# Kernel tuning notes

Hardware: AMD Instinct MI355X
Metric: run time of the kernel (lower is better)

The kernel has to match this reference:

```python
import jax, jax.numpy as jnp
import numpy as np

B = 4096
N_WIRES = 4
N_OPS = 8
# fixed (control, target) wire pairs for the 8 'random' two-qubit CRY gates
PAIRS = [(0, 1), (1, 2), (2, 3), (3, 0), (0, 2), (1, 3), (2, 0), (3, 1)]
AX = "abcd"  # einsum letters for the 4 qubit axes


def _cry(theta):
    """Controlled-RY gate as a [2,2,2,2] tensor (c_out, t_out, c_in, t_in). Real-valued."""
    c, s = jnp.cos(theta / 2), jnp.sin(theta / 2)
    ry = jnp.stack([jnp.stack([c, -s]), jnp.stack([s, c])])  # [2,2]
    G = jnp.zeros((2, 2, 2, 2), dtype=ry.dtype)
    G = G.at[0, :, 0, :].set(jnp.eye(2, dtype=ry.dtype))
    G = G.at[1, :, 1, :].set(ry)
    return G


def _apply_2q(state, G, c, t):
    """Apply 2-qubit gate G to qubits (c, t) of state [N,2,2,2,2]."""
    out = list(AX)
    out[c], out[t] = "x", "y"
    spec = f"xy{AX[c]}{AX[t]},n{AX}->n{''.join(out)}"
    return jnp.einsum(spec, G, state)


def _quanv(x, theta):
    """Batched 4-qubit state-vector sim over all 196 2x2 patches at once."""
    bsz = x.shape[0]
    img = x.reshape(bsz, 28, 28)
    # [B,14,14,2,2] patches; flatten row-major gives [x[r,c], x[r,c+1], x[r+1,c], x[r+1,c+1]]
    patches = img.reshape(bsz, 14, 2, 14, 2).transpose(0, 1, 3, 2, 4)
    angles = patches.reshape(bsz * 196, 4)  # [N,4] RY angles
    # RY(theta)|0> = cos(t/2)|0> + sin(t/2)|1>  -> product state over 4 wires
    amp = jnp.stack([jnp.cos(angles / 2), jnp.sin(angles / 2)], axis=-1)  # [N,4,2]
    state = jnp.einsum("na,nb,nc,nd->nabcd", amp[:, 0], amp[:, 1], amp[:, 2], amp[:, 3])
    # 8 fixed-pattern parameterized CRY gates (RandomLayer analogue; all-real so state stays real)
    for k, (cw, tw) in enumerate(PAIRS):
        state = _apply_2q(state, _cry(theta[k]), cw, tw)
    probs = state ** 2  # real amplitudes -> |amp|^2
    z = jnp.array([1.0, -1.0], dtype=state.dtype)
    meas = jnp.stack([jnp.einsum(f"n{AX},{AX[w]}->n", probs, z) for w in range(N_WIRES)], axis=-1)
    return meas.reshape(bsz, 196 * 4)  # [B,784], patch-major layout matches torch cat


def setup_inputs() -> dict:
    key = jax.random.key(0)
    ks = jax.random.split(key, 11)
    x = jax.random.uniform(ks[0], (B, 1, 28, 28), dtype=jnp.float32)
    theta = jax.random.uniform(ks[1], (N_OPS,), dtype=jnp.float32, minval=0.0, maxval=2.0 * np.pi)
    s = 0.05
    W1 = jax.random.normal(ks[2], (784, 512), jnp.float32) * s
    b1 = jnp.zeros((512,), jnp.float32)
    W2 = jax.random.normal(ks[3], (512, 32), jnp.float32) * s
    b2 = jnp.zeros((32,), jnp.float32)
    W3 = jax.random.normal(ks[4], (32, 512), jnp.float32) * s
    b3 = jnp.zeros((512,), jnp.float32)
    W4 = jax.random.normal(ks[5], (512, 784), jnp.float32) * s
    b4 = jnp.zeros((784,), jnp.float32)
    return dict(x=x, theta=theta, W1=W1, b1=b1, W2=W2, b2=b2, W3=W3, b3=b3, W4=W4, b4=b4)


def reference(x, theta, W1, b1, W2, b2, W3, b3, W4, b4):
    feats = _quanv(x, theta)                          # [B,784]
    h = jax.nn.relu(feats @ W1 + b1)                  # encoder
    latent = h @ W2 + b2                              # [B,32]
    h2 = jax.nn.relu(latent @ W3 + b3)                # decoder
    recon = jax.nn.sigmoid(h2 @ W4 + b4)              # [B,784]
    return recon.reshape(x.shape[0], 1, 28, 28)
```

## Files before the change

### kernel.cpp

```cpp
#include <hip/hip_runtime.h>
#include <hip/hip_bf16.h>
#include <math.h>


#define BATCH   4096
#define NPATCH  196
#define FEATDIM 784
#define KP1     896
#define NP4     832

typedef __bf16 b8 __attribute__((ext_vector_type(8)));
typedef float  f4 __attribute__((ext_vector_type(4)));

__device__ __forceinline__ unsigned short f2bf(float f) {
    unsigned u = __float_as_uint(f);
    u += 0x7FFF + ((u >> 16) & 1);
    return (unsigned short)(u >> 16);
}

__device__ __forceinline__ void gload16(const void* g, void* l) {
    __builtin_amdgcn_global_load_lds(
        (const __attribute__((address_space(1))) unsigned int*)g,
        (__attribute__((address_space(3))) unsigned int*)l, 16, 0, 0);
}

#define Q_END   3136
#define T1_END  3248
#define T4_END  3352
#define FW_END  4376
#define FB_END  4378
#define ZF_END  4602

__global__ __launch_bounds__(256)
void prep_kernel(const float* __restrict__ x, const float* __restrict__ theta,
                 const float* __restrict__ W1, const float* __restrict__ W2,
                 const float* __restrict__ W3, const float* __restrict__ W4,
                 const float* __restrict__ b2, const float* __restrict__ b3,
                 unsigned short* __restrict__ featsB,
                 unsigned short* __restrict__ W1B,
                 unsigned short* __restrict__ W4B,
                 unsigned short* __restrict__ WcT,
                 float* __restrict__ bc) {
    __shared__ float shm[64 * 65];
    const int bid = blockIdx.x;
    const int tid = threadIdx.x;

    if (bid < Q_END) {
        float (*Us)[16] = (float (*)[16])shm;
        if (tid < 16) {
            const int cb[8] = {3, 2, 1, 0, 3, 2, 1, 0};
            const int tb[8] = {2, 1, 0, 3, 1, 0, 3, 2};
            float v[16];
#pragma unroll
            for (int s = 0; s < 16; ++s) v[s] = (s == tid) ? 1.0f : 0.0f;
            for (int k = 0; k < 8; ++k) {
                float th = theta[k] * 0.5f;
                float ct, st;
                __sincosf(th, &st, &ct);
                int cm = 1 << cb[k], tm = 1 << tb[k];
#pragma unroll
                for (int s = 0; s < 16; ++s) {
                    if ((s & cm) && !(s & tm)) {
                        float v0 = v[s], v1 = v[s | tm];
                        v[s]      = ct * v0 - st * v1;
                        v[s | tm] = st * v0 + ct * v1;
                    }
                }
            }
#pragma unroll
            for (int s = 0; s < 16; ++s) Us[s][tid] = v[s];
        }
        __syncthreads();

        int n = bid * 256 + tid;
        int b = n / NPATCH;
        int p = n % NPATCH;
        int r = p / 14;
        int c = p % 14;

        const float* img = x + (size_t)b * FEATDIM;
        float2 p0 = *(const float2*)&img[(2 * r) * 28 + 2 * c];
        float2 p1 = *(const float2*)&img[(2 * r + 1) * 28 + 2 * c];

        float amp[4][2];
        __sincosf(p0.x * 0.5f, &amp[0][1], &amp[0][0]);
        __sincosf(p0.y * 0.5f, &amp[1][1], &amp[1][0]);
        __sincosf(p1.x * 0.5f, &amp[2][1], &amp[2][0]);
        __sincosf(p1.y * 0.5f, &amp[3][1], &amp[3][0]);

        float av[16];
#pragma unroll
        for (int s = 0; s < 16; ++s)
            av[s] = amp[0][(s >> 3) & 1] * amp[1][(s >> 2) & 1] *
                    amp[2][(s >> 1) & 1] * amp[3][s & 1];

        float m0 = 0.f, m1 = 0.f, m2 = 0.f, m3 = 0.f;
#pragma unroll
        for (int s = 0; s < 16; ++s) {
            float vv = 0.f;
#pragma unroll
            for (int t = 0; t < 16; ++t) vv += Us[s][t] * av[t];
            float pr = vv * vv;
            m0 += ((s >> 3) & 1) ? -pr : pr;
            m1 += ((s >> 2) & 1) ? -pr : pr;
            m2 += ((s >> 1) & 1) ? -pr : pr;
            m3 += (s & 1)        ? -pr : pr;
        }
        ushort4 o;
        o.x = f2bf(m0); o.y = f2bf(m1); o.z = f2bf(m2); o.w = f2bf(m3);
        *(ushort4*)&featsB[(size_t)b * KP1 + p * 4] = o;
    } else if (bid < T1_END) {
        float (*T)[65] = (float (*)[65])shm;
        int bb = bid - Q_END;
        int k0 = (bb / 8) * 64, n0 = (bb % 8) * 64;
        int rr = tid >> 6, c = tid & 63;
#pragma unroll
        for (int i = 0; i < 16; ++i) {
            int r = i * 4 + rr;
            if (k0 + r < FEATDIM) T[r][c] = W1[(size_t)(k0 + r) * 512 + n0 + c];
        }
        __syncthreads();
#pragma unroll
        for (int i = 0; i < 16; ++i) {
            int nn = i * 4 + rr;
            unsigned short v = (k0 + c < FEATDIM) ? f2bf(T[c][nn]) : (unsigned short)0;
            W1B[(size_t)(n0 + nn) * KP1 + k0 + c] = v;
        }
    } else if (bid < T4_END) {
        float (*T)[65] = (float (*)[65])shm;
        int bb = bid - T1_END;
        int k0 = (bb / 13) * 64, n0 = (bb % 13) * 64;
        int rr = tid >> 6, c = tid & 63;
#pragma unroll
        for (int i = 0; i < 16; ++i) {
            int r = i * 4 + rr;
            T[r][c] = (n0 + c < FEATDIM) ? W4[(size_t)(k0 + r) * FEATDIM + n0 + c] : 0.f;
        }
        __syncthreads();
#pragma unroll
        for (int i = 0; i < 16; ++i) {
            int nn = i * 4 + rr;
            W4B[(size_t)(n0 + nn) * 512 + k0 + c] = f2bf(T[c][nn]);
        }
    } else if (bid < FW_END) {
        int idx = (bid - T4_END) * 256 + tid;
        int n = idx >> 9, k = idx & 511;
        float s = 0.f;
#pragma unroll
        for (int i = 0; i < 32; ++i) s += W2[k * 32 + i] * W3[i * 512 + n];
        WcT[idx] = f2bf(s);
    } else if (bid < FB_END) {
        int n = (bid - FW_END) * 256 + tid;
        if (n < 512) {
            float s = b3[n];
#pragma unroll
            for (int i = 0; i < 32; ++i) s += b2[i] * W3[i * 512 + n];
            bc[n] = s;
        }
    } else {
        int idx = (bid - FB_END) * 256 + tid;
        int row = idx / 14, j = idx % 14;
        *(float4*)&featsB[(size_t)row * KP1 + FEATDIM + j * 8] =
            make_float4(0.f, 0.f, 0.f, 0.f);
    }
}

template <int ACT, int OUT_BF16>
__global__ __launch_bounds__(256)
void gemm_mfma(const unsigned short* __restrict__ A,
               const unsigned short* __restrict__ BT,
               const float* __restrict__ bias,
               void* __restrict__ C,
               int lda, int ldb, int ldc, int Nlog, int nkt, int gx) {
    __shared__ __align__(16) unsigned short As[2][2][64 * 64];
    __shared__ __align__(16) unsigned short Bs[2][2][64 * 64];

    const int nwg = gridDim.x;
    const int d   = blockIdx.x;
    const int tile = (d & 7) * (nwg >> 3) + (d >> 3);
    const int bx = tile % gx;
    const int by = tile / gx;

    const int t  = threadIdx.x;
    const int w  = t >> 6;
    const int l  = t & 63;
    const int wm = w >> 1;
    const int wn = w & 1;
    const int row0 = by * 64;
    const int col0 = bx * 64;

    const int sr = l >> 3;
    const int sc = ((l & 7) ^ sr) * 8;
    const unsigned short* Ab = A  + (size_t)(row0 + w * 8 + sr) * lda + sc;
    const unsigned short* Bb = BT + (size_t)(col0 + w * 8 + sr) * ldb + sc;

    const int q  = l >> 4;
    const int lx = l & 15;
    const int sx = l & 7;
    const int coff[2] = { ((0 + q) ^ sx) * 16, ((4 + q) ^ sx) * 16 };

    f4 acc[2][2];
#pragma unroll
    for (int m = 0; m < 2; ++m)
#pragma unroll
        for (int n = 0; n < 2; ++n) acc[m][n] = (f4)0.f;

    auto stage = [&](int bi, int kt) {
#pragma unroll
        for (int h = 0; h < 2; ++h) {
            const size_t k0 = (size_t)kt * 128 + h * 64;
            char* la = (char*)&As[bi][h][0] + w * 1024;
            char* lb = (char*)&Bs[bi][h][0] + w * 1024;
            gload16(Ab + k0, la);
            gload16(Bb + k0, lb);
            gload16(Ab + (size_t)32 * lda + k0, la + 4096);
            gload16(Bb + (size_t)32 * ldb + k0, lb + 4096);
        }
    };

    auto compute = [&](int bi) {
#pragma unroll
        for (int h = 0; h < 2; ++h) {
            const char* la = (const char*)&As[bi][h][0];
            const char* lb = (const char*)&Bs[bi][h][0];
#pragma unroll
            for (int kk = 0; kk < 2; ++kk) {
                const int co = coff[kk];
                b8 a[2], bf[2];
#pragma unroll
                for (int m = 0; m < 2; ++m)
                    a[m] = *(const b8*)(la + (wm * 32 + m * 16 + lx) * 128 + co);
#pragma unroll
                for (int n = 0; n < 2; ++n)
                    bf[n] = *(const b8*)(lb + (wn * 32 + n * 16 + lx) * 128 + co);
#pragma unroll
                for (int m = 0; m < 2; ++m)
#pragma unroll
                    for (int n = 0; n < 2; ++n)
                        acc[m][n] = __builtin_amdgcn_mfma_f32_16x16x32_bf16(
                            a[m], bf[n], acc[m][n], 0, 0, 0);
            }
        }
    };

    stage(0, 0);
    __syncthreads();
    for (int kt = 0; kt < nkt; ++kt) {
        if (kt + 1 < nkt) stage((kt + 1) & 1, kt + 1);
        compute(kt & 1);
        __syncthreads();
    }

#pragma unroll
    for (int n = 0; n < 2; ++n) {
        int col = col0 + wn * 32 + n * 16 + lx;
        if (col >= Nlog) continue;
        float bv = bias[col];
#pragma unroll
        for (int m = 0; m < 2; ++m) {
            int row = row0 + wm * 32 + m * 16 + q * 4;
#pragma unroll
            for (int r = 0; r < 4; ++r) {
                float v = acc[m][n][r] + bv;
                if (ACT == 1) v = fmaxf(v, 0.f);
                if (ACT == 2) v = 1.0f / (1.0f + __expf(-v));
                if (OUT_BF16)
                    ((unsigned short*)C)[(size_t)(row + r) * ldc + col] = f2bf(v);
                else
                    __builtin_nontemporal_store(
                        v, &((float*)C)[(size_t)(row + r) * ldc + col]);
            }
        }
    }
}

extern "C" void kernel_launch(void* const* d_in, const int* in_sizes, int n_in,
                              void* d_out, int out_size, void* d_ws, size_t ws_size,
                              hipStream_t stream) {
    const float* x     = (const float*)d_in[0];
    const float* theta = (const float*)d_in[1];
    const float* W1    = (const float*)d_in[2];
    const float* b1    = (const float*)d_in[3];
    const float* W2    = (const float*)d_in[4];
    const float* b2    = (const float*)d_in[5];
    const float* W3    = (const float*)d_in[6];
    const float* b3    = (const float*)d_in[7];
    const float* W4    = (const float*)d_in[8];
    const float* b4    = (const float*)d_in[9];
    float* out = (float*)d_out;

    char* ws = (char*)d_ws;
    unsigned short* featsB = (unsigned short*)ws;   ws += (size_t)BATCH * KP1 * 2;
    unsigned short* W1B    = (unsigned short*)ws;   ws += (size_t)512 * KP1 * 2;
    unsigned short* W4B    = (unsigned short*)ws;   ws += (size_t)NP4 * 512 * 2;
    unsigned short* WcT    = (unsigned short*)ws;   ws += (size_t)512 * 512 * 2;
    float*          bc     = (float*)ws;            ws += 2048;
    unsigned short* h1B    = (unsigned short*)ws;   ws += (size_t)BATCH * 512 * 2;
    unsigned short* h2B    = (unsigned short*)ws;

    prep_kernel<<<ZF_END, 256, 0, stream>>>(
        x, theta, W1, W2, W3, W4, b2, b3, featsB, W1B, W4B, WcT, bc);

    gemm_mfma<1, 1><<<512, 256, 0, stream>>>(
        featsB, W1B, b1, h1B, KP1, KP1, 512, 512, KP1 / 128, 8);
    gemm_mfma<1, 1><<<512, 256, 0, stream>>>(
        h1B, WcT, bc, h2B, 512, 512, 512, 512, 4, 8);
    gemm_mfma<2, 0><<<832, 256, 0, stream>>>(
        h2B, W4B, b4, out, 512, 512, FEATDIM, FEATDIM, 4, 13);
}
```

Baseline: 55.03 us.

## Replace folded W2·W3 GEMM with fused low-rank two-stage mid-layer kernel

Stops precomputing the combined 512x512 weight (W2·W3) and the folded bias, and instead runs the encoder-latent and decoder-first layers as a single fused kernel through the 32-wide latent. Each block computes a 64-row latent tile with MFMA, keeps it in LDS, and multiplies by W3 staged in LDS to produce the ReLU'd h2 directly. This cuts middle-layer FLOPs and prep work, but launches only 64 blocks, which may underutilize the GPU. The latent is also now rounded to bf16.

```diff
diff --git a/kernel.cpp b/kernel.cpp
--- a/kernel.cpp
+++ b/kernel.cpp
@@ -27,20 +27,19 @@
 #define Q_END   3136
 #define T1_END  3248
 #define T4_END  3352
-#define FW_END  4376
-#define FB_END  4378
-#define ZF_END  4602
+#define W2T_END 3416
+#define W3T_END 3480
+#define ZF_END  3704
 
 __global__ __launch_bounds__(256)
 void prep_kernel(const float* __restrict__ x, const float* __restrict__ theta,
                  const float* __restrict__ W1, const float* __restrict__ W2,
                  const float* __restrict__ W3, const float* __restrict__ W4,
-                 const float* __restrict__ b2, const float* __restrict__ b3,
                  unsigned short* __restrict__ featsB,
                  unsigned short* __restrict__ W1B,
                  unsigned short* __restrict__ W4B,
-                 unsigned short* __restrict__ WcT,
-                 float* __restrict__ bc) {
+                 unsigned short* __restrict__ W2T,
+                 unsigned short* __restrict__ W3T) {
     __shared__ float shm[64 * 65];
     const int bid = blockIdx.x;
     const int tid = threadIdx.x;
@@ -142,23 +141,16 @@
             int nn = i * 4 + rr;
             W4B[(size_t)(n0 + nn) * 512 + k0 + c] = f2bf(T[c][nn]);
         }
-    } else if (bid < FW_END) {
+    } else if (bid < W2T_END) {
         int idx = (bid - T4_END) * 256 + tid;
         int n = idx >> 9, k = idx & 511;
-        float s = 0.f;
-#pragma unroll
-        for (int i = 0; i < 32; ++i) s += W2[k * 32 + i] * W3[i * 512 + n];
-        WcT[idx] = f2bf(s);
-    } else if (bid < FB_END) {
-        int n = (bid - FW_END) * 256 + tid;
-        if (n < 512) {
-            float s = b3[n];
-#pragma unroll
-            for (int i = 0; i < 32; ++i) s += b2[i] * W3[i * 512 + n];
-            bc[n] = s;
-        }
+        W2T[idx] = f2bf(W2[(size_t)k * 32 + n]);
+    } else if (bid < W3T_END) {
+        int idx = (bid - W2T_END) * 256 + tid;
+        int n = idx >> 5, k = idx & 31;
+        W3T[idx] = f2bf(W3[(size_t)k * 512 + n]);
     } else {
-        int idx = (bid - FB_END) * 256 + tid;
+        int idx = (bid - W3T_END) * 256 + tid;
         int row = idx / 14, j = idx % 14;
         *(float4*)&featsB[(size_t)row * KP1 + FEATDIM + j * 8] =
             make_float4(0.f, 0.f, 0.f, 0.f);
@@ -270,6 +262,100 @@
                     __builtin_nontemporal_store(
                         v, &((float*)C)[(size_t)(row + r) * ldc + col]);
             }
+        }
+    }
+}
+
+__global__ __launch_bounds__(256)
+void mlp_mid(const unsigned short* __restrict__ h1B,
+             const unsigned short* __restrict__ W2T,
+             const unsigned short* __restrict__ W3T,
+             const float* __restrict__ b2,
+             const float* __restrict__ b3,
+             unsigned short* __restrict__ h2B) {
+    __shared__ __align__(16) unsigned short As[2][64 * 64];
+    __shared__ __align__(16) unsigned short Bs[2][32 * 64];
+    __shared__ __align__(16) unsigned short W3s[512 * 32];
+    __shared__ __align__(16) unsigned short lats[64 * 32];
+
+    const int t  = threadIdx.x;
+    const int w  = t >> 6;
+    const int l  = t & 63;
+    const int q  = l >> 4;
+    const int lx = l & 15;
+    const int sx = l & 7;
+    const int row0 = blockIdx.x * 64;
+
+    {
+        const char* w3g = (const char*)W3T;
+        char* w3l = (char*)W3s;
+#pragma unroll
+        for (int i = 0; i < 8; ++i)
+            gload16(w3g + i * 4096 + w * 1024 + l * 16, w3l + i * 4096 + w * 1024);
+    }
+
+    const int sr = l >> 3;
+    const int sc = ((l & 7) ^ sr) * 8;
+    const unsigned short* Ab = h1B + (size_t)(row0 + w * 8 + sr) * 512 + sc;
+    const unsigned short* Bb = W2T + (size_t)(w * 8 + sr) * 512 + sc;
+
+    const int coff[2] = { ((0 + q) ^ sx) * 16, ((4 + q) ^ sx) * 16 };
+    const float b2v[2] = { b2[lx], b2[16 + lx] };
+
+    f4 acc[2];
+    acc[0] = (f4)0.f;
+    acc[1] = (f4)0.f;
+
+    auto stage = [&](int bi, int kt) {
+        const size_t k0 = (size_t)kt * 64;
+        char* la = (char*)&As[bi][0] + w * 1024;
+        char* lb = (char*)&Bs[bi][0] + w * 1024;
+        gload16(Ab + k0, la);
+        gload16(Ab + (size_t)32 * 512 + k0, la + 4096);
+        gload16(Bb + k0, lb);
+    };
+
+    auto compute = [&](int bi) {
+        const char* la = (const char*)&As[bi][0];
+        const char* lb = (const char*)&Bs[bi][0];
+#pragma unroll
+        for (int kk = 0; kk < 2; ++kk) {
+            const int co = coff[kk];
+            b8 a = *(const b8*)(la + (w * 16 + lx) * 128 + co);
+            b8 bf0 = *(const b8*)(lb + (lx) * 128 + co);
+            b8 bf1 = *(const b8*)(lb + (16 + lx) * 128 + co);
+            acc[0] = __builtin_amdgcn_mfma_f32_16x16x32_bf16(a, bf0, acc[0], 0, 0, 0);
+            acc[1] = __builtin_amdgcn_mfma_f32_16x16x32_bf16(a, bf1, acc[1], 0, 0, 0);
+        }
+    };
+
+    stage(0, 0);
+    __syncthreads();
+    for (int kt = 0; kt < 8; ++kt) {
+        if (kt + 1 < 8) stage((kt + 1) & 1, kt + 1);
+        compute(kt & 1);
+        __syncthreads();
+    }
+
+#pragma unroll
+    for (int n = 0; n < 2; ++n)
+#pragma unroll
+        for (int r = 0; r < 4; ++r)
+            lats[(w * 16 + q * 4 + r) * 32 + n * 16 + lx] =
+                f2bf(acc[n][r] + b2v[n]);
+    __syncthreads();
+
+    b8 a2 = *(const b8*)((const char*)lats + (w * 16 + lx) * 64 + q * 16);
+#pragma unroll
+    for (int j = 0; j < 32; ++j) {
+        b8 bf = *(const b8*)((const char*)W3s + (j * 16 + lx) * 64 + q * 16);
+        f4 o = __builtin_amdgcn_mfma_f32_16x16x32_bf16(a2, bf, (f4)0.f, 0, 0, 0);
+        int col = j * 16 + lx;
+        float bb = b3[col];
+#pragma unroll
+        for (int r = 0; r < 4; ++r) {
+            float v = fmaxf(o[r] + bb, 0.f);
+            h2B[(size_t)(row0 + w * 16 + q * 4 + r) * 512 + col] = f2bf(v);
         }
     }
 }
@@ -293,18 +379,17 @@
     unsigned short* featsB = (unsigned short*)ws;   ws += (size_t)BATCH * KP1 * 2;
     unsigned short* W1B    = (unsigned short*)ws;   ws += (size_t)512 * KP1 * 2;
     unsigned short* W4B    = (unsigned short*)ws;   ws += (size_t)NP4 * 512 * 2;
-    unsigned short* WcT    = (unsigned short*)ws;   ws += (size_t)512 * 512 * 2;
-    float*          bc     = (float*)ws;            ws += 2048;
+    unsigned short* W2T    = (unsigned short*)ws;   ws += (size_t)32 * 512 * 2;
+    unsigned short* W3T    = (unsigned short*)ws;   ws += (size_t)512 * 32 * 2;
     unsigned short* h1B    = (unsigned short*)ws;   ws += (size_t)BATCH * 512 * 2;
     unsigned short* h2B    = (unsigned short*)ws;
 
     prep_kernel<<<ZF_END, 256, 0, stream>>>(
-        x, theta, W1, W2, W3, W4, b2, b3, featsB, W1B, W4B, WcT, bc);
+        x, theta, W1, W2, W3, W4, featsB, W1B, W4B, W2T, W3T);
 
     gemm_mfma<1, 1><<<512, 256, 0, stream>>>(
         featsB, W1B, b1, h1B, KP1, KP1, 512, 512, KP1 / 128, 8);
-    gemm_mfma<1, 1><<<512, 256, 0, stream>>>(
-        h1B, WcT, bc, h2B, 512, 512, 512, 512, 4, 8);
+    mlp_mid<<<64, 256, 0, stream>>>(h1B, W2T, W3T, b2, b3, h2B);
     gemm_mfma<2, 0><<<832, 256, 0, stream>>>(
         h2B, W4B, b4, out, 512, 512, FEATDIM, FEATDIM, 4, 13);
 }
```

New measurement: 56.12 us. About the same (+2.0%).
